# Performance work log

Measured on AMD Instinct MI355X. Metric: run time of the kernel, lower is better.

The kernel has to match this reference:

```python
import jax, jax.numpy as jnp
import numpy as np

LN_EPS = 1e-5
B, T, H = 32, 1024, 1024


def _layer_norm(v, g, b):
    m = v.mean(-1, keepdims=True)
    var = ((v - m) ** 2).mean(-1, keepdims=True)
    return (v - m) / jnp.sqrt(var + LN_EPS) * g + b


def setup_inputs() -> dict:
    key = jax.random.key(0)
    ks = jax.random.split(key, 10)
    s_t = 1.0 / np.sqrt(T)
    s_h = 1.0 / np.sqrt(H)
    return {
        "x": jax.random.normal(ks[0], (B, T, H), jnp.float32),
        # temporal MLP (square T x T, triangular-masked), torch Linear layout [out, in]
        "tw1": jax.random.uniform(ks[1], (T, T), jnp.float32, -s_t, s_t),
        "tb1": jax.random.uniform(ks[2], (T,), jnp.float32, -s_t, s_t),
        "tw2": jax.random.uniform(ks[3], (T, T), jnp.float32, -s_t, s_t),
        "tb2": jax.random.uniform(ks[4], (T,), jnp.float32, -s_t, s_t),
        # channel MLP (square H x H)
        "cw1": jax.random.uniform(ks[5], (H, H), jnp.float32, -s_h, s_h),
        "cb1": jax.random.uniform(ks[6], (H,), jnp.float32, -s_h, s_h),
        "cw2": jax.random.uniform(ks[7], (H, H), jnp.float32, -s_h, s_h),
        "cb2": jax.random.uniform(ks[8], (H,), jnp.float32, -s_h, s_h),
        # LayerNorm affine params
        "ln1_g": jnp.ones((H,), jnp.float32),
        "ln1_b": jnp.zeros((H,), jnp.float32),
        "ln2_g": jnp.ones((H,), jnp.float32),
        "ln2_b": jnp.zeros((H,), jnp.float32),
    }


def reference(x, tw1, tb1, tw2, tb2, cw1, cb1, cw2, cb2, ln1_g, ln1_b, ln2_g, ln2_b):
    t = tw1.shape[0]
    mask = jnp.tril(jnp.ones((t, t), x.dtype))  # diagonal=0: include self
    # temporal mixing: LN -> swap -> masked Linear -> GELU -> masked Linear -> swap
    y = _layer_norm(x, ln1_g, ln1_b)
    y = jnp.swapaxes(y, 1, 2)  # [B, H, T]
    y = y @ (mask * tw1).T + tb1
    y = jax.nn.gelu(y, approximate=False)
    y = y @ (mask * tw2).T + tb2
    y = jnp.swapaxes(y, 1, 2)  # [B, T, H]
    x = x + y
    # channel mixing: LN -> Linear -> GELU -> Linear
    y2 = _layer_norm(x, ln2_g, ln2_b)
    y2 = jax.nn.gelu(y2 @ cw1.T + cb1, approximate=False) @ cw2.T + cb2
    return x + y2
```

## Files before the change

kernel.cpp:

```cpp
#include <hip/hip_runtime.h>
#include <hip/hip_bf16.h>

#define BDIM 32
#define TDIM 1024
#define HDIM 1024

typedef __attribute__((ext_vector_type(8))) short short8;
typedef __attribute__((ext_vector_type(8))) unsigned short ushort8;
typedef __attribute__((ext_vector_type(4))) unsigned short u16x4;
typedef __attribute__((ext_vector_type(4))) float f32x4;

__device__ __forceinline__ unsigned short f2b(float f){
  unsigned u = __float_as_uint(f);
  u += 0x7fffu + ((u>>16)&1u);
  return (unsigned short)(u>>16);
}
__device__ __forceinline__ float gelu_f(float v){ return 0.5f*v*(1.0f+erff(v*0.70710678118f)); }
__device__ __forceinline__ void stv(float* p, float v){ *p = v; }
__device__ __forceinline__ void stv(unsigned short* p, float v){ *p = f2b(v); }

__global__ void prep_weights(const float* __restrict__ w1, const float* __restrict__ w2,
                             const float* __restrict__ c1, const float* __restrict__ c2,
                             unsigned short* __restrict__ w1m, unsigned short* __restrict__ w2m,
                             unsigned short* __restrict__ c1b, unsigned short* __restrict__ c2b){
  int idx = blockIdx.x*blockDim.x + threadIdx.x;
  int e = idx*4;
  int i = e >> 10, j0 = e & 1023;
  f32x4 a = *(const f32x4*)(w1+e);
  f32x4 b = *(const f32x4*)(w2+e);
  f32x4 c = *(const f32x4*)(c1+e);
  f32x4 d = *(const f32x4*)(c2+e);
  u16x4 av, bv, cv, dv;
  #pragma unroll
  for (int q=0;q<4;++q){
    float am = (j0+q <= i) ? a[q] : 0.f;
    float bm = (j0+q <= i) ? b[q] : 0.f;
    av[q]=f2b(am); bv[q]=f2b(bm); cv[q]=f2b(c[q]); dv[q]=f2b(d[q]);
  }
  *(u16x4*)(w1m+e)=av; *(u16x4*)(w2m+e)=bv; *(u16x4*)(c1b+e)=cv; *(u16x4*)(c2b+e)=dv;
}

__global__ __launch_bounds__(256) void ln1_stats_transpose(
    const float* __restrict__ x, const float* __restrict__ g, const float* __restrict__ bta,
    unsigned short* __restrict__ xnT){
  __shared__ float sm[64], sr[64];
  __shared__ float tile[64][65];
  const int t0 = blockIdx.x*64;
  const int b  = blockIdx.y;
  const int tid = threadIdx.x, wid = tid>>6, lane = tid&63;
  const size_t base = (size_t)b*TDIM*HDIM;
  for (int rr=0; rr<16; ++rr){
    int r = rr*4 + wid;
    const float* pr = x + base + (size_t)(t0+r)*HDIM;
    float s=0.f, s2=0.f;
    #pragma unroll
    for (int it=0; it<4; ++it){
      f32x4 v = *(const f32x4*)(pr + it*256 + lane*4);
      #pragma unroll
      for (int c=0;c<4;++c){ s += v[c]; s2 += v[c]*v[c]; }
    }
    #pragma unroll
    for (int off=32; off>0; off>>=1){ s += __shfl_xor(s,off,64); s2 += __shfl_xor(s2,off,64); }
    if (lane==0){
      float m = s * (1.0f/HDIM);
      sm[r] = m; sr[r] = rsqrtf(s2*(1.0f/HDIM) - m*m + 1e-5f);
    }
  }
  __syncthreads();
  const int rr = tid>>3, c8 = tid&7;
  for (int ht=0; ht<16; ++ht){
    int h0 = ht*64;
    #pragma unroll
    for (int p=0;p<2;++p){
      int r = rr + p*32;
      float m = sm[r], rs = sr[r];
      f32x4 v0 = *(const f32x4*)(x + base + (size_t)(t0+r)*HDIM + h0 + c8*8);
      f32x4 v1 = *(const f32x4*)(x + base + (size_t)(t0+r)*HDIM + h0 + c8*8 + 4);
      #pragma unroll
      for (int c=0;c<4;++c){
        int h = c8*8+c;
        tile[r][h]   = (v0[c]-m)*rs*g[h0+h]   + bta[h0+h];
        tile[r][h+4] = (v1[c]-m)*rs*g[h0+h+4] + bta[h0+h+4];
      }
    }
    __syncthreads();
    #pragma unroll
    for (int p=0;p<2;++p){
      int hr = rr + p*32;
      ushort8 ov;
      #pragma unroll
      for (int c=0;c<8;++c) ov[c] = f2b(tile[c8*8+c][hr]);
      *(ushort8*)(xnT + base + (size_t)(h0+hr)*TDIM + t0 + c8*8) = ov;
    }
    __syncthreads();
  }
}

__global__ void ln_fused(const float* __restrict__ p, const float* __restrict__ g,
                         const float* __restrict__ bta, unsigned short* __restrict__ o){
  int wid = threadIdx.x>>6, lane = threadIdx.x&63;
  size_t row = (size_t)blockIdx.x*4 + wid;
  const float* pr = p + row*HDIM;
  f32x4 v[4];
  float s=0.f, s2=0.f;
  #pragma unroll
  for (int it=0; it<4; ++it){
    v[it] = *(const f32x4*)(pr + it*256 + lane*4);
    #pragma unroll
    for (int c=0;c<4;++c){ s += v[it][c]; s2 += v[it][c]*v[it][c]; }
  }
  #pragma unroll
  for (int off=32; off>0; off>>=1){ s += __shfl_xor(s,off,64); s2 += __shfl_xor(s2,off,64); }
  float m = s * (1.0f/HDIM);
  float rs = rsqrtf(s2*(1.0f/HDIM) - m*m + 1e-5f);
  #pragma unroll
  for (int it=0; it<4; ++it){
    int h0 = it*256 + lane*4;
    f32x4 gg = *(const f32x4*)(g + h0);
    f32x4 bb = *(const f32x4*)(bta + h0);
    u16x4 ov;
    #pragma unroll
    for (int c=0;c<4;++c) ov[c] = f2b((v[it][c]-m)*rs*gg[c] + bb[c]);
    *(u16x4*)(o + row*HDIM + h0) = ov;
  }
}

template<int MODE, typename CT>
__global__ __launch_bounds__(256)
void gemm_k(const unsigned short* __restrict__ act, const unsigned short* __restrict__ wgt,
            CT* __restrict__ C, const float* __restrict__ bias, const float* __restrict__ resid){
  const int bid = blockIdx.x;
  const int tile = (bid & 7)*256 + (bid >> 3);
  const int panel = tile >> 3;
  const int inner = tile & 7;
  const unsigned short *pa, *pb;
  size_t cbase; int rg0, cg0; int kend;
  if constexpr (MODE==1){
    int b = panel>>3, mt = panel&7;
    pa = act + (size_t)b*1048576 + (size_t)mt*131072;
    pb = wgt + (size_t)inner*131072;
    kend = (inner+1)*128;
    cbase = (size_t)b*1048576; rg0 = mt*128; cg0 = inner*128;
  } else if constexpr (MODE==2){
    int b = panel>>3, nt = panel&7;
    pa = wgt + (size_t)inner*131072;
    pb = act + (size_t)b*1048576 + (size_t)nt*131072;
    kend = (inner+1)*128;
    cbase = (size_t)b*1048576; rg0 = inner*128; cg0 = nt*128;
  } else {
    pa = act + (size_t)panel*131072;
    pb = wgt + (size_t)inner*131072;
    kend = 1024;
    cbase = 0; rg0 = panel*128; cg0 = inner*128;
  }
  __shared__ short As[128*32];
  __shared__ short Bs[128*32];
  const int tid = threadIdx.x;
  const int lane = tid & 63, wid = tid >> 6;
  const int wr = wid >> 1, wc = wid & 1;
  f32x4 acc[4][4];
  #pragma unroll
  for (int i=0;i<4;++i)
    #pragma unroll
    for (int j=0;j<4;++j) acc[i][j] = (f32x4)(0.f);
  const int aoff = (wr*64 + (lane&15))*32 + (lane>>4)*8;
  const int boff = (wc*64 + (lane&15))*32 + (lane>>4)*8;
  const int L0 = tid*16;

  for (int k0=0; k0<kend; k0+=32){
    __syncthreads();
    #pragma unroll
    for (int q=0;q<2;++q){
      int L = L0 + q*4096;
      int row = L >> 6;
      int ke  = (L & 63) >> 1;
      __builtin_amdgcn_global_load_lds(
        (const __attribute__((address_space(1))) void*)(pa + (size_t)row*1024 + k0 + ke),
        (__attribute__((address_space(3))) void*)((char*)As + L), 16, 0, 0);
      __builtin_amdgcn_global_load_lds(
        (const __attribute__((address_space(1))) void*)(pb + (size_t)row*1024 + k0 + ke),
        (__attribute__((address_space(3))) void*)((char*)Bs + L), 16, 0, 0);
    }
    __syncthreads();
    short8 af[4], bfv[4];
    #pragma unroll
    for (int i=0;i<4;++i){
      af[i]  = *(const short8*)(As + aoff + i*16*32);
      bfv[i] = *(const short8*)(Bs + boff + i*16*32);
    }
    #pragma unroll
    for (int i=0;i<4;++i)
      #pragma unroll
      for (int j=0;j<4;++j)
        acc[i][j] = __builtin_amdgcn_mfma_f32_16x16x32_bf16(af[i], bfv[j], acc[i][j], 0,0,0);
  }

  #pragma unroll
  for (int i=0;i<4;++i){
    int rbase = rg0 + wr*64 + i*16 + ((lane>>4)<<2);
    #pragma unroll
    for (int j=0;j<4;++j){
      int cg = cg0 + wc*64 + j*16 + (lane&15);
      float bn = (MODE!=2) ? bias[cg] : 0.f;
      #pragma unroll
      for (int r=0;r<4;++r){
        int rg = rbase + r;
        float v = acc[i][j][r];
        if (MODE==1 || MODE==3){ v += bn; v = gelu_f(v); }
        else if (MODE==2){ v += bias[rg]; v += resid[cbase + (size_t)rg*1024 + cg]; }
        else { v += bn; v += resid[cbase + (size_t)rg*1024 + cg]; }
        stv(&C[cbase + (size_t)rg*1024 + cg], v);
      }
    }
  }
}

extern "C" void kernel_launch(void* const* d_in, const int* in_sizes, int n_in,
                              void* d_out, int out_size, void* d_ws, size_t ws_size,
                              hipStream_t stream){
  const float* x    = (const float*)d_in[0];
  const float* tw1  = (const float*)d_in[1];
  const float* tb1  = (const float*)d_in[2];
  const float* tw2  = (const float*)d_in[3];
  const float* tb2  = (const float*)d_in[4];
  const float* cw1  = (const float*)d_in[5];
  const float* cb1  = (const float*)d_in[6];
  const float* cw2  = (const float*)d_in[7];
  const float* cb2  = (const float*)d_in[8];
  const float* g1   = (const float*)d_in[9];
  const float* bb1  = (const float*)d_in[10];
  const float* g2   = (const float*)d_in[11];
  const float* bb2  = (const float*)d_in[12];
  float* out = (float*)d_out;

  char* ws = (char*)d_ws;
  unsigned short* bufA = (unsigned short*)(ws);
  unsigned short* bufB = (unsigned short*)(ws + 67108864);
  unsigned short* w1m  = (unsigned short*)(ws + 134217728);
  unsigned short* w2m  = (unsigned short*)(ws + 136314880);
  unsigned short* c1b  = (unsigned short*)(ws + 138412032);
  unsigned short* c2b  = (unsigned short*)(ws + 140509184);

  prep_weights<<<1024,256,0,stream>>>(tw1,tw2,cw1,cw2,w1m,w2m,c1b,c2b);
  ln1_stats_transpose<<<dim3(16,32),256,0,stream>>>(x, g1, bb1, bufA);
  gemm_k<1,unsigned short><<<2048,256,0,stream>>>(bufA, w1m, bufB, tb1, nullptr);
  gemm_k<2,float><<<2048,256,0,stream>>>(bufB, w2m, out, tb2, x);
  ln_fused<<<8192,256,0,stream>>>(out, g2, bb2, bufA);
  gemm_k<3,unsigned short><<<2048,256,0,stream>>>(bufA, c1b, bufB, cb1, nullptr);
  gemm_k<4,float><<<2048,256,0,stream>>>(bufB, c2b, out, cb2, out);
}
```

Measured before the change: 557.1 us.

## Use 256x256 double-buffered GEMM tiles and a bf16 intermediate residual

Replaces the 128x128 single-buffered GEMM with a 512-thread kernel that computes 256x256 output tiles. Each block stages a 64-wide K slice into 128KB of dynamic LDS and double-buffers it, so the next slice loads while MFMAs run on the current one. The intermediate x after temporal mixing is now stored as bf16, which halves the traffic for the second LayerNorm and the final residual read. The trade-offs are fewer blocks in flight, heavy LDS use per block, and extra rounding error on the residual path.

```diff
diff --git a/kernel.cpp b/kernel.cpp
--- a/kernel.cpp
+++ b/kernel.cpp
@@ -10,6 +10,7 @@
 typedef __attribute__((ext_vector_type(4))) unsigned short u16x4;
 typedef __attribute__((ext_vector_type(4))) float f32x4;
 
+__device__ __forceinline__ float b2f(unsigned short h){ return __uint_as_float(((unsigned)h)<<16); }
 __device__ __forceinline__ unsigned short f2b(float f){
   unsigned u = __float_as_uint(f);
   u += 0x7fffu + ((u>>16)&1u);
@@ -96,108 +97,119 @@
   }
 }
 
-__global__ void ln_fused(const float* __restrict__ p, const float* __restrict__ g,
+__global__ void ln_fused(const unsigned short* __restrict__ p, const float* __restrict__ g,
                          const float* __restrict__ bta, unsigned short* __restrict__ o){
   int wid = threadIdx.x>>6, lane = threadIdx.x&63;
   size_t row = (size_t)blockIdx.x*4 + wid;
-  const float* pr = p + row*HDIM;
-  f32x4 v[4];
+  const unsigned short* pr = p + row*HDIM + lane*16;
+  ushort8 v0 = *(const ushort8*)(pr);
+  ushort8 v1 = *(const ushort8*)(pr+8);
+  float f[16];
   float s=0.f, s2=0.f;
   #pragma unroll
-  for (int it=0; it<4; ++it){
-    v[it] = *(const f32x4*)(pr + it*256 + lane*4);
-    #pragma unroll
-    for (int c=0;c<4;++c){ s += v[it][c]; s2 += v[it][c]*v[it][c]; }
-  }
+  for (int c=0;c<8;++c){ f[c]=b2f(v0[c]); f[c+8]=b2f(v1[c]); }
+  #pragma unroll
+  for (int c=0;c<16;++c){ s += f[c]; s2 += f[c]*f[c]; }
   #pragma unroll
   for (int off=32; off>0; off>>=1){ s += __shfl_xor(s,off,64); s2 += __shfl_xor(s2,off,64); }
   float m = s * (1.0f/HDIM);
   float rs = rsqrtf(s2*(1.0f/HDIM) - m*m + 1e-5f);
-  #pragma unroll
-  for (int it=0; it<4; ++it){
-    int h0 = it*256 + lane*4;
-    f32x4 gg = *(const f32x4*)(g + h0);
-    f32x4 bb = *(const f32x4*)(bta + h0);
-    u16x4 ov;
-    #pragma unroll
-    for (int c=0;c<4;++c) ov[c] = f2b((v[it][c]-m)*rs*gg[c] + bb[c]);
-    *(u16x4*)(o + row*HDIM + h0) = ov;
-  }
-}
-
-template<int MODE, typename CT>
-__global__ __launch_bounds__(256)
-void gemm_k(const unsigned short* __restrict__ act, const unsigned short* __restrict__ wgt,
-            CT* __restrict__ C, const float* __restrict__ bias, const float* __restrict__ resid){
+  int h0 = lane*16;
+  ushort8 o0, o1;
+  #pragma unroll
+  for (int c=0;c<8;++c){
+    o0[c] = f2b((f[c]-m)*rs*g[h0+c] + bta[h0+c]);
+    o1[c] = f2b((f[c+8]-m)*rs*g[h0+c+8] + bta[h0+c+8]);
+  }
+  *(ushort8*)(o + row*HDIM + h0) = o0;
+  *(ushort8*)(o + row*HDIM + h0 + 8) = o1;
+}
+
+template<int MODE, typename CT, typename RT>
+__global__ __launch_bounds__(512,2)
+void gemm256(const unsigned short* __restrict__ act, const unsigned short* __restrict__ wgt,
+             CT* __restrict__ C, const float* __restrict__ bias, const RT* __restrict__ resid){
+  extern __shared__ short S[];
   const int bid = blockIdx.x;
-  const int tile = (bid & 7)*256 + (bid >> 3);
-  const int panel = tile >> 3;
-  const int inner = tile & 7;
+  const int tile = (bid & 7)*64 + (bid >> 3);
+  const int panel = tile >> 2;
+  const int inner = tile & 3;
   const unsigned short *pa, *pb;
-  size_t cbase; int rg0, cg0; int kend;
+  size_t cbase; int rg0, cg0, kend;
   if constexpr (MODE==1){
-    int b = panel>>3, mt = panel&7;
-    pa = act + (size_t)b*1048576 + (size_t)mt*131072;
-    pb = wgt + (size_t)inner*131072;
-    kend = (inner+1)*128;
-    cbase = (size_t)b*1048576; rg0 = mt*128; cg0 = inner*128;
+    int b = panel>>2, mt = panel&3;
+    pa = act + (size_t)b*1048576 + (size_t)mt*262144;
+    pb = wgt + (size_t)inner*262144;
+    kend = (inner+1)*256;
+    cbase = (size_t)b*1048576; rg0 = mt*256; cg0 = inner*256;
   } else if constexpr (MODE==2){
-    int b = panel>>3, nt = panel&7;
-    pa = wgt + (size_t)inner*131072;
-    pb = act + (size_t)b*1048576 + (size_t)nt*131072;
-    kend = (inner+1)*128;
-    cbase = (size_t)b*1048576; rg0 = inner*128; cg0 = nt*128;
+    int b = panel>>2, nt = panel&3;
+    pa = wgt + (size_t)inner*262144;
+    pb = act + (size_t)b*1048576 + (size_t)nt*262144;
+    kend = (inner+1)*256;
+    cbase = (size_t)b*1048576; rg0 = inner*256; cg0 = nt*256;
   } else {
-    pa = act + (size_t)panel*131072;
-    pb = wgt + (size_t)inner*131072;
+    pa = act + (size_t)panel*262144;
+    pb = wgt + (size_t)inner*262144;
     kend = 1024;
-    cbase = 0; rg0 = panel*128; cg0 = inner*128;
-  }
-  __shared__ short As[128*32];
-  __shared__ short Bs[128*32];
+    cbase = 0; rg0 = panel*256; cg0 = inner*256;
+  }
   const int tid = threadIdx.x;
   const int lane = tid & 63, wid = tid >> 6;
-  const int wr = wid >> 1, wc = wid & 1;
-  f32x4 acc[4][4];
-  #pragma unroll
-  for (int i=0;i<4;++i)
+  const int wr = wid >> 2, wc = wid & 3;
+  f32x4 acc[8][4];
+  #pragma unroll
+  for (int i=0;i<8;++i)
     #pragma unroll
     for (int j=0;j<4;++j) acc[i][j] = (f32x4)(0.f);
-  const int aoff = (wr*64 + (lane&15))*32 + (lane>>4)*8;
-  const int boff = (wc*64 + (lane&15))*32 + (lane>>4)*8;
-  const int L0 = tid*16;
-
-  for (int k0=0; k0<kend; k0+=32){
-    __syncthreads();
-    #pragma unroll
-    for (int q=0;q<2;++q){
-      int L = L0 + q*4096;
-      int row = L >> 6;
-      int ke  = (L & 63) >> 1;
+
+  const int NT = kend >> 6;
+  const int Lb = tid*16;
+  auto STAGE = [&](int buf, int k0){
+    #pragma unroll
+    for (int l=0;l<4;++l){
+      int L = Lb + l*8192;
+      int row = L >> 7;
+      int ke  = (L & 127) >> 1;
       __builtin_amdgcn_global_load_lds(
         (const __attribute__((address_space(1))) void*)(pa + (size_t)row*1024 + k0 + ke),
-        (__attribute__((address_space(3))) void*)((char*)As + L), 16, 0, 0);
+        (__attribute__((address_space(3))) void*)((char*)S + buf*32768 + L), 16, 0, 0);
       __builtin_amdgcn_global_load_lds(
         (const __attribute__((address_space(1))) void*)(pb + (size_t)row*1024 + k0 + ke),
-        (__attribute__((address_space(3))) void*)((char*)Bs + L), 16, 0, 0);
+        (__attribute__((address_space(3))) void*)((char*)S + 65536 + buf*32768 + L), 16, 0, 0);
+    }
+  };
+
+  const int arow = (wr*128 + (lane&15))*64 + (lane>>4)*8;
+  const int brow = (wc*64  + (lane&15))*64 + (lane>>4)*8;
+
+  STAGE(0, 0);
+  __syncthreads();
+  int cur = 0;
+  for (int t=0; t<NT; ++t){
+    if (t+1 < NT) STAGE(cur^1, (t+1)<<6);
+    const short* Sa = S + cur*16384;
+    const short* Sb = S + 32768 + cur*16384;
+    #pragma unroll
+    for (int s=0;s<2;++s){
+      short8 af[8], bfv[4];
+      #pragma unroll
+      for (int i=0;i<8;++i) af[i] = *(const short8*)(Sa + arow + s*32 + i*1024);
+      #pragma unroll
+      for (int j=0;j<4;++j) bfv[j] = *(const short8*)(Sb + brow + s*32 + j*1024);
+      #pragma unroll
+      for (int i=0;i<8;++i)
+        #pragma unroll
+        for (int j=0;j<4;++j)
+          acc[i][j] = __builtin_amdgcn_mfma_f32_16x16x32_bf16(af[i], bfv[j], acc[i][j], 0,0,0);
     }
     __syncthreads();
-    short8 af[4], bfv[4];
-    #pragma unroll
-    for (int i=0;i<4;++i){
-      af[i]  = *(const short8*)(As + aoff + i*16*32);
-      bfv[i] = *(const short8*)(Bs + boff + i*16*32);
-    }
-    #pragma unroll
-    for (int i=0;i<4;++i)
-      #pragma unroll
-      for (int j=0;j<4;++j)
-        acc[i][j] = __builtin_amdgcn_mfma_f32_16x16x32_bf16(af[i], bfv[j], acc[i][j], 0,0,0);
-  }
-
-  #pragma unroll
-  for (int i=0;i<4;++i){
-    int rbase = rg0 + wr*64 + i*16 + ((lane>>4)<<2);
+    cur ^= 1;
+  }
+
+  #pragma unroll
+  for (int i=0;i<8;++i){
+    int rbase = rg0 + wr*128 + i*16 + ((lane>>4)<<2);
     #pragma unroll
     for (int j=0;j<4;++j){
       int cg = cg0 + wc*64 + j*16 + (lane&15);
@@ -208,7 +220,7 @@
         float v = acc[i][j][r];
         if (MODE==1 || MODE==3){ v += bn; v = gelu_f(v); }
         else if (MODE==2){ v += bias[rg]; v += resid[cbase + (size_t)rg*1024 + cg]; }
-        else { v += bn; v += resid[cbase + (size_t)rg*1024 + cg]; }
+        else { v += bn; v += b2f(resid[cbase + (size_t)rg*1024 + cg]); }
         stv(&C[cbase + (size_t)rg*1024 + cg], v);
       }
     }
@@ -236,16 +248,17 @@
   char* ws = (char*)d_ws;
   unsigned short* bufA = (unsigned short*)(ws);
   unsigned short* bufB = (unsigned short*)(ws + 67108864);
-  unsigned short* w1m  = (unsigned short*)(ws + 134217728);
-  unsigned short* w2m  = (unsigned short*)(ws + 136314880);
-  unsigned short* c1b  = (unsigned short*)(ws + 138412032);
-  unsigned short* c2b  = (unsigned short*)(ws + 140509184);
+  unsigned short* xmid = (unsigned short*)(ws + 134217728);
+  unsigned short* w1m  = (unsigned short*)(ws + 201326592);
+  unsigned short* w2m  = (unsigned short*)(ws + 203423744);
+  unsigned short* c1b  = (unsigned short*)(ws + 205520896);
+  unsigned short* c2b  = (unsigned short*)(ws + 207618048);
 
   prep_weights<<<1024,256,0,stream>>>(tw1,tw2,cw1,cw2,w1m,w2m,c1b,c2b);
   ln1_stats_transpose<<<dim3(16,32),256,0,stream>>>(x, g1, bb1, bufA);
-  gemm_k<1,unsigned short><<<2048,256,0,stream>>>(bufA, w1m, bufB, tb1, nullptr);
-  gemm_k<2,float><<<2048,256,0,stream>>>(bufB, w2m, out, tb2, x);
-  ln_fused<<<8192,256,0,stream>>>(out, g2, bb2, bufA);
-  gemm_k<3,unsigned short><<<2048,256,0,stream>>>(bufA, c1b, bufB, cb1, nullptr);
-  gemm_k<4,float><<<2048,256,0,stream>>>(bufB, c2b, out, cb2, out);
-}
+  gemm256<1,unsigned short,float><<<512,512,131072,stream>>>(bufA, w1m, bufB, tb1, (const float*)nullptr);
+  gemm256<2,unsigned short,float><<<512,512,131072,stream>>>(bufB, w2m, xmid, tb2, x);
+  ln_fused<<<8192,256,0,stream>>>(xmid, g2, bb2, bufA);
+  gemm256<3,unsigned short,unsigned short><<<512,512,131072,stream>>>(bufA, c1b, bufB, cb1, (const unsigned short*)nullptr);
+  gemm256<4,float,unsigned short><<<512,512,131072,stream>>>(bufB, c2b, out, cb2, xmid);
+}
```

Result: faster. 526.3 us (-5.5%).
